# Kernel optimization log

Hardware: AMD Instinct MI355X
Metric: run time of the kernel (lower is better)

## Reference

```python
import jax, jax.numpy as jnp
import numpy as np

DIM = 256
HEADS = 8
WSZ = (2, 7, 7)
SSZ = (1, 3, 3)
EPS = 1e-5


def _rel_index(wsz):
    wt, wh, ww = wsz
    coords = np.stack(np.meshgrid(np.arange(wt), np.arange(wh), np.arange(ww), indexing='ij'))
    coords = coords.reshape(3, -1)  # (3, N)
    rel = coords[:, :, None] - coords[:, None, :]  # (3, N, N)
    rel = rel.transpose(1, 2, 0).copy()  # (N, N, 3)
    rel[:, :, 0] += wt - 1
    rel[:, :, 1] += wh - 1
    rel[:, :, 2] += ww - 1
    rel[:, :, 0] *= (2 * wh - 1) * (2 * ww - 1)
    rel[:, :, 1] *= (2 * ww - 1)
    return rel.sum(-1)  # (N, N) int


def _attn_mask_np(T, H, W, wsz, ssz):
    wt, wh, ww = wsz
    st, sh, sw = ssz
    img = np.zeros((T, H, W), np.int32)
    cnt = 0
    for t in (slice(0, -wt), slice(-wt, -st), slice(-st, None)):
        for h in (slice(0, -wh), slice(-wh, -sh), slice(-sh, None)):
            for w in (slice(0, -ww), slice(-ww, -sw), slice(-sw, None)):
                img[t, h, w] = cnt
                cnt += 1
    m = img.reshape(T // wt, wt, H // wh, wh, W // ww, ww)
    m = m.transpose(0, 2, 4, 1, 3, 5).reshape(-1, wt * wh * ww)  # (nW, N)
    diff = m[:, :, None] - m[:, None, :]
    return np.where(diff != 0, -100.0, 0.0).astype(np.float32)  # (nW, N, N)


def _ln(x, w, b):
    mu = x.mean(-1, keepdims=True)
    var = jnp.mean((x - mu) ** 2, -1, keepdims=True)
    return (x - mu) * jax.lax.rsqrt(var + EPS) * w + b


def _window_partition(x, wsz):
    B, T, H, W, C = x.shape
    wt, wh, ww = wsz
    x = x.reshape(B, T // wt, wt, H // wh, wh, W // ww, ww, C)
    x = x.transpose(0, 1, 3, 5, 2, 4, 6, 7)
    return x.reshape(-1, wt * wh * ww, C)


def _window_reverse(xw, wsz, B, T, H, W):
    wt, wh, ww = wsz
    C = xw.shape[-1]
    x = xw.reshape(B, T // wt, H // wh, W // ww, wt, wh, ww, C)
    x = x.transpose(0, 1, 4, 2, 5, 3, 6, 7)
    return x.reshape(B, T, H, W, C)


def setup_inputs() -> dict:
    key = jax.random.key(0)
    ks = jax.random.split(key, 8)
    B, T, H, W = 2, 8, 56, 56
    d = DIM
    hid = 4 * d
    rpe_rows = (2 * WSZ[0] - 1) * (2 * WSZ[1] - 1) * (2 * WSZ[2] - 1)
    s = 0.02
    return {
        'x': jax.random.normal(ks[0], (B, T, H, W, d), jnp.float32),
        'norm1_w': jnp.ones((d,), jnp.float32),
        'norm1_b': jnp.zeros((d,), jnp.float32),
        'qkv_w': jax.random.normal(ks[1], (3 * d, d), jnp.float32) * s,
        'qkv_b': jnp.zeros((3 * d,), jnp.float32),
        'proj_w': jax.random.normal(ks[2], (d, d), jnp.float32) * s,
        'proj_b': jnp.zeros((d,), jnp.float32),
        'rpe_table': jax.random.normal(ks[3], (rpe_rows, HEADS), jnp.float32) * s,
        'norm2_w': jnp.ones((d,), jnp.float32),
        'norm2_b': jnp.zeros((d,), jnp.float32),
        'fc1_w': jax.random.normal(ks[4], (hid, d), jnp.float32) * s,
        'fc1_b': jnp.zeros((hid,), jnp.float32),
        'fc2_w': jax.random.normal(ks[5], (d, hid), jnp.float32) * s,
        'fc2_b': jnp.zeros((d,), jnp.float32),
    }


def reference(x, norm1_w, norm1_b, qkv_w, qkv_b, proj_w, proj_b, rpe_table,
              norm2_w, norm2_b, fc1_w, fc1_b, fc2_w, fc2_b):
    B, T, H, W, C = x.shape
    wt, wh, ww = WSZ
    N = wt * wh * ww
    hd = C // HEADS
    scale = hd ** -0.5

    shortcut = x
    h = _ln(x, norm1_w, norm1_b)
    # shifted branch: cyclic roll + mask
    h = jnp.roll(h, (-SSZ[0], -SSZ[1], -SSZ[2]), axis=(1, 2, 3))
    mask = jnp.asarray(_attn_mask_np(T, H, W, WSZ, SSZ))  # (nW, N, N)
    nW = mask.shape[0]

    xw = _window_partition(h, WSZ)  # (B*nW, N, C)
    Bw = xw.shape[0]

    qkv = xw @ qkv_w.T + qkv_b  # (Bw, N, 3C)
    qkv = qkv.reshape(Bw, N, 3, HEADS, hd).transpose(2, 0, 3, 1, 4)
    q, k, v = qkv[0], qkv[1], qkv[2]  # (Bw, H, N, hd)

    idx = _rel_index(WSZ)  # (N, N)
    bias = rpe_table[idx].transpose(2, 0, 1)  # (heads, N, N)

    attn = jnp.einsum('bhnd,bhmd->bhnm', q * scale, k) + bias[None]
    attn = attn.reshape(B, nW, HEADS, N, N) + mask[None, :, None]
    attn = jax.nn.softmax(attn, axis=-1).reshape(Bw, HEADS, N, N)

    out = jnp.einsum('bhnm,bhmd->bhnd', attn, v)
    out = out.transpose(0, 2, 1, 3).reshape(Bw, N, C)
    out = out @ proj_w.T + proj_b

    out = _window_reverse(out, WSZ, B, T, H, W)
    out = jnp.roll(out, (SSZ[0], SSZ[1], SSZ[2]), axis=(1, 2, 3))

    x = shortcut + out
    h2 = _ln(x, norm2_w, norm2_b)
    h2 = jax.nn.gelu(h2 @ fc1_w.T + fc1_b, approximate=False)
    h2 = h2 @ fc2_w.T + fc2_b
    return x + h2
```

## Files before the change

### kernel.cpp

```cpp
#include <hip/hip_runtime.h>
#include <math.h>

#define TOKENS 50176
#define NWIN   512
#define C_DIM  256

typedef __attribute__((ext_vector_type(8))) short short8;
typedef __attribute__((ext_vector_type(4))) float f32x4;

__device__ __forceinline__ unsigned short f2bf(float f) {
    unsigned int u = __builtin_bit_cast(unsigned int, f);
    u += 0x7fffu + ((u >> 16) & 1);
    return (unsigned short)(u >> 16);
}

__device__ __forceinline__ void gll16(const void* g, void* l) {
    __builtin_amdgcn_global_load_lds(
        (const __attribute__((address_space(1))) unsigned int*)g,
        (__attribute__((address_space(3))) unsigned int*)l, 16, 0, 0);
}

__device__ __forceinline__ float gelu_exact(float v) {
    float z  = v * 0.70710678118654752f;
    float az = fabsf(z);
    float t  = __builtin_amdgcn_rcpf(1.f + 0.3275911f * az);
    float p  = ((((1.061405429f * t - 1.453152027f) * t + 1.421413741f) * t
                 - 0.284496736f) * t + 0.254829592f) * t;
    float er = 1.f - p * __expf(-az * az);
    er = (z < 0.f) ? -er : er;
    return 0.5f * v * (1.f + er);
}

__device__ __forceinline__ int win_token_to_flat(int u) {
    int g = u / 98;
    int n = u - g * 98;
    int bb  = g >> 8;
    int rem = g & 255;
    int tb = rem >> 6, hb = (rem >> 3) & 7, wb = rem & 7;
    int dt = n / 49;
    int r2 = n - dt * 49;
    int dh = r2 / 7, dw = r2 - dh * 7;
    int t = tb * 2 + dt, h = hb * 7 + dh, w = wb * 7 + dw;
    int ts = (t + 1) & 7;
    int hs = h + 3; if (hs >= 56) hs -= 56;
    int wsx = w + 3; if (wsx >= 56) wsx -= 56;
    return ((bb * 8 + ts) * 56 + hs) * 56 + wsx;
}

__global__ __launch_bounds__(256) void cvt_all_kernel(
        const float* __restrict__ s0, const float* __restrict__ s1,
        const float* __restrict__ s2, const float* __restrict__ s3,
        unsigned short* __restrict__ d0, unsigned short* __restrict__ d1,
        unsigned short* __restrict__ d2, unsigned short* __restrict__ d3) {
    int i = blockIdx.x * 256 + threadIdx.x;
    if (i < 196608)      d0[i] = f2bf(s0[i]);
    else if (i < 262144) d1[i - 196608] = f2bf(s1[i - 196608]);
    else if (i < 524288) d2[i - 262144] = f2bf(s2[i - 262144]);
    else                 d3[i - 524288] = f2bf(s3[i - 524288]);
}

__global__ __launch_bounds__(256) void bm_kernel(
        const float* __restrict__ rpe, float* __restrict__ bm) {
    int i = blockIdx.x * 256 + threadIdx.x;
    int c  = i % 112;
    int t1 = i / 112;
    int r  = t1 % 112;
    int t2 = t1 / 112;
    int head = t2 & 7;
    int cls  = t2 >> 3;
    float val;
    if (c >= 98) {
        val = -1e30f;
    } else if (r >= 98) {
        val = 0.f;
    } else {
        int dt = r / 49, rr = r - dt * 49, dh = rr / 7, dw = rr - dh * 7;
        int dt2 = c / 49, cc = c - dt2 * 49, dh2 = cc / 7, dw2 = cc - dh2 * 7;
        int rt  = (cls & 4) ? (dt  == 0 ? 1 : 2) : 0;
        int rh  = (cls & 2) ? (dh  <  4 ? 1 : 2) : 0;
        int rw  = (cls & 1) ? (dw  <  4 ? 1 : 2) : 0;
        int rt2 = (cls & 4) ? (dt2 == 0 ? 1 : 2) : 0;
        int rh2 = (cls & 2) ? (dh2 <  4 ? 1 : 2) : 0;
        int rw2 = (cls & 1) ? (dw2 <  4 ? 1 : 2) : 0;
        int reg1 = rt * 9 + rh * 3 + rw, reg2 = rt2 * 9 + rh2 * 3 + rw2;
        int idx = (dt - dt2 + 1) * 169 + (dh - dh2 + 6) * 13 + (dw - dw2 + 6);
        val = rpe[idx * 8 + head] + ((reg1 == reg2) ? 0.f : -100.f);
    }
    bm[i] = val;
}

template<bool GATHER>
__global__ __launch_bounds__(256) void ln_kernel(
        const float* __restrict__ x, const float* __restrict__ w,
        const float* __restrict__ b, unsigned short* __restrict__ out) {
    int token = blockIdx.x * 4 + (threadIdx.x >> 6);
    int lane  = threadIdx.x & 63;
    size_t so = GATHER ? (size_t)win_token_to_flat(token) * C_DIM
                       : (size_t)token * C_DIM;
    const float* src = x + so;
    float v[4];
    float sum = 0.f;
#pragma unroll
    for (int j = 0; j < 4; ++j) { v[j] = src[lane + 64 * j]; sum += v[j]; }
#pragma unroll
    for (int o = 32; o > 0; o >>= 1) sum += __shfl_xor(sum, o, 64);
    float mu = sum * (1.f / 256.f);
    float var = 0.f;
#pragma unroll
    for (int j = 0; j < 4; ++j) { float d = v[j] - mu; var += d * d; }
#pragma unroll
    for (int o = 32; o > 0; o >>= 1) var += __shfl_xor(var, o, 64);
    float rstd = rsqrtf(var * (1.f / 256.f) + 1e-5f);
    unsigned short* dst = out + (size_t)token * C_DIM;
#pragma unroll
    for (int j = 0; j < 4; ++j) {
        int c = lane + 64 * j;
        dst[c] = f2bf((v[j] - mu) * rstd * w[c] + b[c]);
    }
}

template<int EPI>
__global__ __launch_bounds__(256) void mfma_gemm(
        const unsigned short* __restrict__ A, const unsigned short* __restrict__ B,
        const float* __restrict__ bias, const float* __restrict__ res,
        void* __restrict__ Cout, int M, int N, int K) {
    __shared__ __attribute__((aligned(16))) unsigned short smem[4][128 * 32];
#define ASMB(b) (smem[(b)])
#define BSMB(b) (smem[2 + (b)])
    int tid = threadIdx.x;
    int wave = tid >> 6, lane = tid & 63;

    int nwg = gridDim.x * gridDim.y;
    int bid = blockIdx.y * gridDim.x + blockIdx.x;
    int swz = (bid & 7) * (nwg >> 3) + (bid >> 3);
    int bx = swz % gridDim.x, by = swz / gridDim.x;

    int row0 = by * 128, col0 = bx * 128;
    int wr = (wave >> 1) * 64;
    int wc = (wave & 1) * 64;

    f32x4 acc[4][4] = {};

    int sr = tid >> 2;
    int sk = (tid & 3) * 8;
    const unsigned short* Ag0 = A + (size_t)(row0 + sr) * K + sk;
    const unsigned short* Ag1 = A + (size_t)(row0 + 64 + sr) * K + sk;
    const unsigned short* Bg0 = B + (size_t)(col0 + sr) * K + sk;
    const unsigned short* Bg1 = B + (size_t)(col0 + 64 + sr) * K + sk;
    int loff = tid * 8;

    int fm = lane & 15, fq = lane >> 4;
    int fks = fq * 8;

    gll16(Ag0, &ASMB(0)[loff]);
    gll16(Ag1, &ASMB(0)[loff + 2048]);
    gll16(Bg0, &BSMB(0)[loff]);
    gll16(Bg1, &BSMB(0)[loff + 2048]);

    int nk = K >> 5;
    for (int s = 0; s < nk; ++s) {
        int cur = s & 1;
        __syncthreads();
        if (s + 1 < nk) {
            int k0 = (s + 1) << 5;
            gll16(Ag0 + k0, &ASMB(cur ^ 1)[loff]);
            gll16(Ag1 + k0, &ASMB(cur ^ 1)[loff + 2048]);
            gll16(Bg0 + k0, &BSMB(cur ^ 1)[loff]);
            gll16(Bg1 + k0, &BSMB(cur ^ 1)[loff + 2048]);
        }
        short8 af[4], bfr[4];
#pragma unroll
        for (int t4 = 0; t4 < 4; ++t4) {
            af[t4]  = *(const short8*)&ASMB(cur)[(wr + t4 * 16 + fm) * 32 + fks];
            bfr[t4] = *(const short8*)&BSMB(cur)[(wc + t4 * 16 + fm) * 32 + fks];
        }
#pragma unroll
        for (int i = 0; i < 4; ++i)
#pragma unroll
            for (int j = 0; j < 4; ++j)
                acc[i][j] = __builtin_amdgcn_mfma_f32_16x16x32_bf16(
                    af[i], bfr[j], acc[i][j], 0, 0, 0);
    }

    int ccol0 = col0 + wc + fm;
    float bj[4];
#pragma unroll
    for (int j = 0; j < 4; ++j) bj[j] = bias[ccol0 + j * 16];

    __syncthreads();

    if (EPI == 0 || EPI == 2) {
        unsigned short* Ls = &smem[0][0];
        float mul = (EPI == 0 && col0 < 256) ? 0.17677669529663687f : 1.f;
#pragma unroll
        for (int i = 0; i < 4; ++i)
#pragma unroll
            for (int v = 0; v < 4; ++v) {
                int lr = wr + i * 16 + fq * 4 + v;
#pragma unroll
                for (int j = 0; j < 4; ++j) {
                    float val = acc[i][j][v] + bj[j];
                    val = (EPI == 2) ? gelu_exact(val) : val * mul;
                    Ls[lr * 128 + wc + j * 16 + fm] = f2bf(val);
                }
            }
        __syncthreads();
        unsigned short* C = (unsigned short*)Cout;
#pragma unroll
        for (int p = 0; p < 8; ++p) {
            int lin = p * 2048 + tid * 8;
            int lr = lin >> 7, lc = lin & 127;
            *(short8*)(C + (size_t)(row0 + lr) * N + col0 + lc) =
                *(const short8*)&Ls[lin];
        }
    } else {
        float* fs = (float*)&smem[0][0];
        float* C = (float*)Cout;
#pragma unroll
        for (int h = 0; h < 2; ++h) {
            if (h) __syncthreads();
            if (wr == h * 64) {
#pragma unroll
                for (int i = 0; i < 4; ++i)
#pragma unroll
                    for (int v = 0; v < 4; ++v) {
                        int lr = i * 16 + fq * 4 + v;
#pragma unroll
                        for (int j = 0; j < 4; ++j)
                            fs[lr * 128 + wc + j * 16 + fm] = acc[i][j][v] + bj[j];
                    }
            }
            __syncthreads();
            int tr = tid >> 2, tcb = (tid & 3) * 32;
            int grow = row0 + h * 64 + tr;
            size_t gbase = (EPI == 1)
                ? (size_t)win_token_to_flat(grow) * C_DIM + col0 + tcb
                : (size_t)grow * N + col0 + tcb;
            const float* rs = res + gbase;
            float* Cp = C + gbase;
            const float* ls = &fs[tr * 128 + tcb];
#pragma unroll
            for (int q = 0; q < 8; ++q) {
                f32x4 r = *(const f32x4*)(rs + q * 4);
                f32x4 a = *(const f32x4*)(ls + q * 4);
                r.x += a.x; r.y += a.y; r.z += a.z; r.w += a.w;
                *(f32x4*)(Cp + q * 4) = r;
            }
        }
    }
#undef ASMB
#undef BSMB
}

__global__ __launch_bounds__(256) void attn_mfma_kernel(
        const unsigned short* __restrict__ qkv, const float* __restrict__ bm,
        unsigned short* __restrict__ out) {
    __shared__ __attribute__((aligned(16))) unsigned short Vt[32][136];
    __shared__ __attribute__((aligned(16))) unsigned short Pw[4][16][136];
    int blk = blockIdx.x;
    int g = blk >> 3, head = blk & 7;
    int tid = threadIdx.x, wave = tid >> 6, lane = tid & 63;

    for (int i = tid; i < 32 * 30; i += 256) {
        int d = i / 30, c = 98 + (i - d * 30);
        Vt[d][c] = 0;
    }
    const unsigned short* vbase = qkv + (size_t)g * 98 * 768 + 512 + head * 32;
    for (int i = tid; i < 98 * 16; i += 256) {
        int n = i >> 4, dp = i & 15;
        unsigned int val = *(const unsigned int*)(vbase + (size_t)n * 768 + dp * 2);
        Vt[dp * 2][n]     = (unsigned short)val;
        Vt[dp * 2 + 1][n] = (unsigned short)(val >> 16);
    }
    {
        int m = lane >> 2, c = 112 + (lane & 3) * 4;
        *(unsigned long long*)&Pw[wave][m][c] = 0ULL;
    }
    __syncthreads();

    const unsigned short* qbase = qkv + (size_t)g * 98 * 768 + head * 32;
    const unsigned short* kbase = qbase + 256;
    int rem = g & 255;
    int cls = (((rem >> 6) == 3) << 2) | (((((rem >> 3) & 7)) == 7) << 1) | ((rem & 7) == 7);
    const float* bmh = bm + (size_t)(cls * 8 + head) * 112 * 112;

    int fm = lane & 15, fq = lane >> 4;
    int fk = fq * 8;
    unsigned short* obase = out + (size_t)g * 98 * 256 + head * 32;

    for (int s = wave; s < 7; s += 4) {
        int m0 = s * 16;
        int arow = m0 + fm; if (arow > 97) arow = 97;
        short8 af = *(const short8*)(qbase + (size_t)arow * 768 + fk);
        f32x4 S[7];
        f32x4 z = {0.f, 0.f, 0.f, 0.f};
#pragma unroll
        for (int j = 0; j < 7; ++j) {
            int krow = j * 16 + fm; if (krow > 97) krow = 97;
            short8 kf = *(const short8*)(kbase + (size_t)krow * 768 + fk);
            S[j] = __builtin_amdgcn_mfma_f32_16x16x32_bf16(af, kf, z, 0, 0, 0);
        }
        const float* bmrow = bmh + (m0 + fq * 4) * 112 + fm;
#pragma unroll
        for (int j = 0; j < 7; ++j)
#pragma unroll
            for (int v = 0; v < 4; ++v)
                S[j][v] += bmrow[v * 112 + j * 16];
        float inv[4];
#pragma unroll
        for (int v = 0; v < 4; ++v) {
            float m_ = S[0][v];
#pragma unroll
            for (int j = 1; j < 7; ++j) m_ = fmaxf(m_, S[j][v]);
#pragma unroll
            for (int o = 1; o < 16; o <<= 1) m_ = fmaxf(m_, __shfl_xor(m_, o, 64));
            float t = 0.f;
#pragma unroll
            for (int j = 0; j < 7; ++j) { S[j][v] = __expf(S[j][v] - m_); t += S[j][v]; }
#pragma unroll
            for (int o = 1; o < 16; o <<= 1) t += __shfl_xor(t, o, 64);
            inv[v] = 1.f / t;
        }
#pragma unroll
        for (int j = 0; j < 7; ++j)
#pragma unroll
            for (int v = 0; v < 4; ++v)
                Pw[wave][fq * 4 + v][j * 16 + fm] = f2bf(S[j][v]);
        f32x4 O0 = {0.f, 0.f, 0.f, 0.f}, O1 = {0.f, 0.f, 0.f, 0.f};
#pragma unroll
        for (int ks = 0; ks < 4; ++ks) {
            short8 pf = *(const short8*)&Pw[wave][fm][ks * 32 + fk];
            short8 v0 = *(const short8*)&Vt[fm][ks * 32 + fk];
            short8 v1 = *(const short8*)&Vt[16 + fm][ks * 32 + fk];
            O0 = __builtin_amdgcn_mfma_f32_16x16x32_bf16(pf, v0, O0, 0, 0, 0);
            O1 = __builtin_amdgcn_mfma_f32_16x16x32_bf16(pf, v1, O1, 0, 0, 0);
        }
#pragma unroll
        for (int v = 0; v < 4; ++v) {
            int row = m0 + fq * 4 + v;
            if (row < 98) {
                obase[(size_t)row * 256 + fm]      = f2bf(O0[v] * inv[v]);
                obase[(size_t)row * 256 + 16 + fm] = f2bf(O1[v] * inv[v]);
            }
        }
    }
}

extern "C" void kernel_launch(void* const* d_in, const int* in_sizes, int n_in,
                              void* d_out, int out_size, void* d_ws, size_t ws_size,
                              hipStream_t stream) {
    const float* x     = (const float*)d_in[0];
    const float* n1w   = (const float*)d_in[1];
    const float* n1b   = (const float*)d_in[2];
    const float* qkvw  = (const float*)d_in[3];
    const float* qkvb  = (const float*)d_in[4];
    const float* projw = (const float*)d_in[5];
    const float* projb = (const float*)d_in[6];
    const float* rpe   = (const float*)d_in[7];
    const float* n2w   = (const float*)d_in[8];
    const float* n2b   = (const float*)d_in[9];
    const float* fc1w  = (const float*)d_in[10];
    const float* fc1b  = (const float*)d_in[11];
    const float* fc2w  = (const float*)d_in[12];
    const float* fc2b  = (const float*)d_in[13];
    float* out = (float*)d_out;

    unsigned short* wqkv  = (unsigned short*)d_ws;
    unsigned short* wproj = wqkv + 768 * 256;
    unsigned short* wfc1  = wproj + 256 * 256;
    unsigned short* wfc2  = wfc1 + 1024 * 256;
    float* bm = (float*)(wfc2 + 256 * 1024);
    unsigned short* actA  = (unsigned short*)(bm + 8 * 8 * 112 * 112);
    unsigned short* attnO = actA + (size_t)TOKENS * 256;
    unsigned short* qkv_bf = attnO + (size_t)TOKENS * 256;
    unsigned short* fc1o = qkv_bf;

    bm_kernel<<<8 * 8 * 112 * 112 / 256, 256, 0, stream>>>(rpe, bm);
    cvt_all_kernel<<<786432 / 256, 256, 0, stream>>>(
        qkvw, projw, fc1w, fc2w, wqkv, wproj, wfc1, wfc2);

    ln_kernel<true><<<TOKENS / 4, 256, 0, stream>>>(x, n1w, n1b, actA);
    mfma_gemm<0><<<dim3(768 / 128, TOKENS / 128), 256, 0, stream>>>(
        actA, wqkv, qkvb, nullptr, qkv_bf, TOKENS, 768, 256);
    attn_mfma_kernel<<<NWIN * 8, 256, 0, stream>>>(qkv_bf, bm, attnO);
    mfma_gemm<1><<<dim3(256 / 128, TOKENS / 128), 256, 0, stream>>>(
        attnO, wproj, projb, x, out, TOKENS, 256, 256);
    ln_kernel<false><<<TOKENS / 4, 256, 0, stream>>>(out, n2w, n2b, actA);
    mfma_gemm<2><<<dim3(1024 / 128, TOKENS / 128), 256, 0, stream>>>(
        actA, wfc1, fc1b, nullptr, fc1o, TOKENS, 1024, 256);
    mfma_gemm<3><<<dim3(256 / 128, TOKENS / 128), 256, 0, stream>>>(
        fc1o, wfc2, fc2b, out, out, TOKENS, 256, 1024);
}
```

Measured before the change: 382.5 us.

## Fuse fc1, GELU and fc2 into one MLP kernel keeping hidden activations in LDS

Replaces the two separate GEMM launches for fc1 (with GELU) and fc2 (with residual) with a single kernel. Each 64-row block computes the 1024-wide hidden layer in chunks of 128 and stores GELU results as bf16 in LDS. It then accumulates the fc2 product in registers and adds bias and residual at the end. This removes the write and re-read of the large bf16 hidden tensor through global memory. In exchange it uses 64-row tiles with a large accumulator set, more LDS, fewer waves per block and less weight reuse per tile. The generic GEMM epilogue is simplified to drop the now-unused EPI 2/3 paths.

```diff
diff --git a/kernel.cpp b/kernel.cpp
--- a/kernel.cpp
+++ b/kernel.cpp
@@ -189,20 +189,17 @@
 
     __syncthreads();
 
-    if (EPI == 0 || EPI == 2) {
+    if (EPI == 0) {
         unsigned short* Ls = &smem[0][0];
-        float mul = (EPI == 0 && col0 < 256) ? 0.17677669529663687f : 1.f;
+        float mul = (col0 < 256) ? 0.17677669529663687f : 1.f;
 #pragma unroll
         for (int i = 0; i < 4; ++i)
 #pragma unroll
             for (int v = 0; v < 4; ++v) {
                 int lr = wr + i * 16 + fq * 4 + v;
 #pragma unroll
-                for (int j = 0; j < 4; ++j) {
-                    float val = acc[i][j][v] + bj[j];
-                    val = (EPI == 2) ? gelu_exact(val) : val * mul;
-                    Ls[lr * 128 + wc + j * 16 + fm] = f2bf(val);
-                }
+                for (int j = 0; j < 4; ++j)
+                    Ls[lr * 128 + wc + j * 16 + fm] = f2bf((acc[i][j][v] + bj[j]) * mul);
             }
         __syncthreads();
         unsigned short* C = (unsigned short*)Cout;
@@ -233,9 +230,7 @@
             __syncthreads();
             int tr = tid >> 2, tcb = (tid & 3) * 32;
             int grow = row0 + h * 64 + tr;
-            size_t gbase = (EPI == 1)
-                ? (size_t)win_token_to_flat(grow) * C_DIM + col0 + tcb
-                : (size_t)grow * N + col0 + tcb;
+            size_t gbase = (size_t)win_token_to_flat(grow) * C_DIM + col0 + tcb;
             const float* rs = res + gbase;
             float* Cp = C + gbase;
             const float* ls = &fs[tr * 128 + tcb];
@@ -250,6 +245,148 @@
     }
 #undef ASMB
 #undef BSMB
+}
+
+__global__ __launch_bounds__(256, 2) void mlp_kernel(
+        const unsigned short* __restrict__ A,
+        const unsigned short* __restrict__ W1,
+        const float* __restrict__ b1,
+        const unsigned short* __restrict__ W2,
+        const float* __restrict__ b2,
+        float* __restrict__ out) {
+    __shared__ __attribute__((aligned(16))) unsigned short L[36864];
+    int tid = threadIdx.x;
+    int wave = tid >> 6, lane = tid & 63;
+    int fm = lane & 15, fq = lane >> 4;
+
+    int nwg = gridDim.x;
+    int bid = blockIdx.x;
+    int swz = (bid & 7) * (nwg >> 3) + (bid >> 3);
+    int r0 = swz * 64;
+
+    int wr  = (wave >> 1) * 32;
+    int wch = wave & 1;
+
+    int srow = tid >> 2, sk = (tid & 3) * 8;
+    const unsigned short* Ag  = A  + (size_t)(r0 + srow) * 256 + sk;
+    const unsigned short* W2s = W2 + (size_t)srow * 1024 + sk;
+
+    f32x4 acc2[2][8] = {};
+
+    for (int nc = 0; nc < 8; ++nc) {
+        const unsigned short* Bg = W1 + (size_t)(nc * 128 + srow) * 256 + sk;
+        float bj1[4];
+#pragma unroll
+        for (int j = 0; j < 4; ++j) bj1[j] = b1[nc * 128 + wch * 64 + j * 16 + fm];
+
+        gll16(Ag, &L[tid * 8]);
+        gll16(Bg, &L[4096 + tid * 8]);
+        gll16(Bg + (size_t)64 * 256, &L[4096 + 2048 + tid * 8]);
+
+        f32x4 acc1[2][4] = {};
+        for (int s = 0; s < 8; ++s) {
+            int cur = s & 1;
+            __syncthreads();
+            if (s + 1 < 8) {
+                int k0 = (s + 1) << 5;
+                gll16(Ag + k0, &L[(cur ^ 1) * 2048 + tid * 8]);
+                gll16(Bg + k0, &L[4096 + (cur ^ 1) * 4096 + tid * 8]);
+                gll16(Bg + (size_t)64 * 256 + k0,
+                      &L[4096 + (cur ^ 1) * 4096 + 2048 + tid * 8]);
+            }
+            short8 af[2], bf[4];
+#pragma unroll
+            for (int i = 0; i < 2; ++i)
+                af[i] = *(const short8*)&L[cur * 2048 + (wr + i * 16 + fm) * 32 + fq * 8];
+#pragma unroll
+            for (int j = 0; j < 4; ++j)
+                bf[j] = *(const short8*)&L[4096 + cur * 4096 +
+                                           (wch * 64 + j * 16 + fm) * 32 + fq * 8];
+#pragma unroll
+            for (int i = 0; i < 2; ++i)
+#pragma unroll
+                for (int j = 0; j < 4; ++j)
+                    acc1[i][j] = __builtin_amdgcn_mfma_f32_16x16x32_bf16(
+                        af[i], bf[j], acc1[i][j], 0, 0, 0);
+        }
+
+        {
+            int kc = nc * 128;
+#pragma unroll
+            for (int p = 0; p < 4; ++p)
+                gll16(W2s + (size_t)p * 64 * 1024 + kc,
+                      &L[20480 + p * 2048 + tid * 8]);
+        }
+#pragma unroll
+        for (int i = 0; i < 2; ++i)
+#pragma unroll
+            for (int v = 0; v < 4; ++v) {
+                int row = wr + i * 16 + fq * 4 + v;
+#pragma unroll
+                for (int j = 0; j < 4; ++j) {
+                    int col = wch * 64 + j * 16 + fm;
+                    float val = gelu_exact(acc1[i][j][v] + bj1[j]);
+                    L[12288 + (col >> 3) * 512 + row * 8 + (col & 7)] = f2bf(val);
+                }
+            }
+        __syncthreads();
+
+        for (int k2 = 0; k2 < 4; ++k2) {
+            int cb = k2 & 1;
+            if (k2) __syncthreads();
+            if (k2 + 1 < 4) {
+                int kc = nc * 128 + (k2 + 1) * 32;
+#pragma unroll
+                for (int p = 0; p < 4; ++p)
+                    gll16(W2s + (size_t)p * 64 * 1024 + kc,
+                          &L[20480 + (cb ^ 1) * 8192 + p * 2048 + tid * 8]);
+            }
+            short8 ha[2], b2f[8];
+#pragma unroll
+            for (int i = 0; i < 2; ++i)
+                ha[i] = *(const short8*)&L[12288 + (k2 * 4 + fq) * 512 +
+                                           (wr + i * 16 + fm) * 8];
+#pragma unroll
+            for (int j = 0; j < 8; ++j)
+                b2f[j] = *(const short8*)&L[20480 + cb * 8192 +
+                                            (wch * 128 + j * 16 + fm) * 32 + fq * 8];
+#pragma unroll
+            for (int i = 0; i < 2; ++i)
+#pragma unroll
+                for (int j = 0; j < 8; ++j)
+                    acc2[i][j] = __builtin_amdgcn_mfma_f32_16x16x32_bf16(
+                        ha[i], b2f[j], acc2[i][j], 0, 0, 0);
+        }
+    }
+
+    float bjo[8];
+#pragma unroll
+    for (int j = 0; j < 8; ++j) bjo[j] = b2[wch * 128 + j * 16 + fm];
+    __syncthreads();
+    float* fs = (float*)L;
+#pragma unroll
+    for (int i = 0; i < 2; ++i)
+#pragma unroll
+        for (int v = 0; v < 4; ++v) {
+            int lr = wr + i * 16 + fq * 4 + v;
+#pragma unroll
+            for (int j = 0; j < 8; ++j)
+                fs[lr * 256 + wch * 128 + j * 16 + fm] = acc2[i][j][v] + bjo[j];
+        }
+    __syncthreads();
+    {
+        int tr = tid >> 2, tcb = (tid & 3) * 64;
+        size_t gb = (size_t)(r0 + tr) * 256 + tcb;
+        const float* ls = &fs[tr * 256 + tcb];
+        float* Cp = out + gb;
+#pragma unroll
+        for (int q = 0; q < 16; ++q) {
+            f32x4 r = *(const f32x4*)(Cp + q * 4);
+            f32x4 a = *(const f32x4*)(ls + q * 4);
+            r.x += a.x; r.y += a.y; r.z += a.z; r.w += a.w;
+            *(f32x4*)(Cp + q * 4) = r;
+        }
+    }
 }
 
 __global__ __launch_bounds__(256) void attn_mfma_kernel(
@@ -373,7 +510,6 @@
     unsigned short* actA  = (unsigned short*)(bm + 8 * 8 * 112 * 112);
     unsigned short* attnO = actA + (size_t)TOKENS * 256;
     unsigned short* qkv_bf = attnO + (size_t)TOKENS * 256;
-    unsigned short* fc1o = qkv_bf;
 
     bm_kernel<<<8 * 8 * 112 * 112 / 256, 256, 0, stream>>>(rpe, bm);
     cvt_all_kernel<<<786432 / 256, 256, 0, stream>>>(
@@ -386,8 +522,6 @@
     mfma_gemm<1><<<dim3(256 / 128, TOKENS / 128), 256, 0, stream>>>(
         attnO, wproj, projb, x, out, TOKENS, 256, 256);
     ln_kernel<false><<<TOKENS / 4, 256, 0, stream>>>(out, n2w, n2b, actA);
-    mfma_gemm<2><<<dim3(1024 / 128, TOKENS / 128), 256, 0, stream>>>(
-        actA, wfc1, fc1b, nullptr, fc1o, TOKENS, 1024, 256);
-    mfma_gemm<3><<<dim3(256 / 128, TOKENS / 128), 256, 0, stream>>>(
-        fc1o, wfc2, fc2b, out, out, TOKENS, 256, 1024);
-}
+    mlp_kernel<<<TOKENS / 64, 256, 0, stream>>>(
+        actA, wfc1, fc1b, wfc2, fc2b, out);
+}
```

New measurement: 396.0 us. 1.04x slower.

## Fuse projection GEMM with residual add and LayerNorm2 in one kernel

Applied to the files above, without the earlier changes.

Replaces the projection GEMM plus separate LayerNorm kernel with a single kernel that computes full 256-column rows per 64-row tile. It adds bias and residual, writes the fp32 output, then computes row mean and variance and writes the normalized bf16 activations. This removes one kernel launch and a full fp32 re-read of the output. The cost is larger per-block tiles, more registers, smaller tiles along M, and a one-pass variance formula that is less numerically robust.

```diff
diff --git a/kernel.cpp b/kernel.cpp
--- a/kernel.cpp
+++ b/kernel.cpp
@@ -6,6 +6,7 @@
 #define C_DIM  256
 
 typedef __attribute__((ext_vector_type(8))) short short8;
+typedef __attribute__((ext_vector_type(4))) short s16x4;
 typedef __attribute__((ext_vector_type(4))) float f32x4;
 
 __device__ __forceinline__ unsigned short f2bf(float f) {
@@ -233,9 +234,7 @@
             __syncthreads();
             int tr = tid >> 2, tcb = (tid & 3) * 32;
             int grow = row0 + h * 64 + tr;
-            size_t gbase = (EPI == 1)
-                ? (size_t)win_token_to_flat(grow) * C_DIM + col0 + tcb
-                : (size_t)grow * N + col0 + tcb;
+            size_t gbase = (size_t)grow * N + col0 + tcb;
             const float* rs = res + gbase;
             float* Cp = C + gbase;
             const float* ls = &fs[tr * 128 + tcb];
@@ -250,6 +249,137 @@
     }
 #undef ASMB
 #undef BSMB
+}
+
+__global__ __launch_bounds__(256) void proj_ln_kernel(
+        const unsigned short* __restrict__ A,
+        const unsigned short* __restrict__ B,
+        const float* __restrict__ bias,
+        const float* __restrict__ res,
+        const float* __restrict__ n2w, const float* __restrict__ n2b,
+        float* __restrict__ out,
+        unsigned short* __restrict__ actA) {
+    __shared__ __attribute__((aligned(16))) unsigned short L[20480];
+    int tid = threadIdx.x;
+    int wave = tid >> 6, lane = tid & 63;
+    int fm = lane & 15, fq = lane >> 4;
+
+    int nwg = gridDim.x;
+    int bid = blockIdx.x;
+    int swz = (bid & 7) * (nwg >> 3) + (bid >> 3);
+    int r0 = swz * 64;
+
+    int wrow = (wave >> 1) * 32;
+    int wcol = (wave & 1) * 128;
+
+    f32x4 acc[2][8] = {};
+
+    int sr = tid >> 2, sk = (tid & 3) * 8;
+    const unsigned short* Ag = A + (size_t)(r0 + sr) * 256 + sk;
+    const unsigned short* Bg = B + (size_t)sr * 256 + sk;
+
+    gll16(Ag, &L[tid * 8]);
+#pragma unroll
+    for (int p = 0; p < 4; ++p)
+        gll16(Bg + (size_t)p * 16384, &L[4096 + p * 2048 + tid * 8]);
+
+    for (int s = 0; s < 8; ++s) {
+        int cur = s & 1;
+        __syncthreads();
+        if (s + 1 < 8) {
+            int k0 = (s + 1) << 5;
+            gll16(Ag + k0, &L[(cur ^ 1) * 2048 + tid * 8]);
+#pragma unroll
+            for (int p = 0; p < 4; ++p)
+                gll16(Bg + (size_t)p * 16384 + k0,
+                      &L[4096 + (cur ^ 1) * 8192 + p * 2048 + tid * 8]);
+        }
+        short8 af[2], bfr[8];
+#pragma unroll
+        for (int i = 0; i < 2; ++i)
+            af[i] = *(const short8*)&L[cur * 2048 + (wrow + i * 16 + fm) * 32 + fq * 8];
+#pragma unroll
+        for (int j = 0; j < 8; ++j)
+            bfr[j] = *(const short8*)&L[4096 + cur * 8192 +
+                                        (wcol + j * 16 + fm) * 32 + fq * 8];
+#pragma unroll
+        for (int i = 0; i < 2; ++i)
+#pragma unroll
+            for (int j = 0; j < 8; ++j)
+                acc[i][j] = __builtin_amdgcn_mfma_f32_16x16x32_bf16(
+                    af[i], bfr[j], acc[i][j], 0, 0, 0);
+    }
+
+    float bj[8];
+#pragma unroll
+    for (int j = 0; j < 8; ++j) bj[j] = bias[wcol + j * 16 + fm];
+
+    __syncthreads();
+
+    float* fs   = (float*)L;
+    float* redu = (float*)&L[16640];
+
+    int tr = tid >> 3;
+    int c0 = (tid & 7) * 4;
+
+#pragma unroll
+    for (int h = 0; h < 2; ++h) {
+        if (h) __syncthreads();
+        if (wrow == h * 32) {
+#pragma unroll
+            for (int i = 0; i < 2; ++i)
+#pragma unroll
+                for (int v = 0; v < 4; ++v) {
+                    int lr = i * 16 + fq * 4 + v;
+#pragma unroll
+                    for (int j = 0; j < 8; ++j)
+                        fs[lr * 260 + wcol + j * 16 + fm] = acc[i][j][v] + bj[j];
+                }
+        }
+        __syncthreads();
+        int flat = win_token_to_flat(r0 + h * 32 + tr);
+        size_t gb = (size_t)flat * 256;
+        float vals[32];
+        float s1 = 0.f, s2 = 0.f;
+#pragma unroll
+        for (int q = 0; q < 8; ++q) {
+            int c = c0 + q * 32;
+            f32x4 rr = *(const f32x4*)(res + gb + c);
+            f32x4 aa = *(const f32x4*)&fs[tr * 260 + c];
+            f32x4 o;
+            o.x = rr.x + aa.x; o.y = rr.y + aa.y;
+            o.z = rr.z + aa.z; o.w = rr.w + aa.w;
+            *(f32x4*)(out + gb + c) = o;
+            vals[q * 4 + 0] = o.x; vals[q * 4 + 1] = o.y;
+            vals[q * 4 + 2] = o.z; vals[q * 4 + 3] = o.w;
+            s1 += o.x + o.y + o.z + o.w;
+            s2 += o.x * o.x + o.y * o.y + o.z * o.z + o.w * o.w;
+        }
+        redu[(tr * 8 + (tid & 7)) * 2 + 0] = s1;
+        redu[(tr * 8 + (tid & 7)) * 2 + 1] = s2;
+        __syncthreads();
+        float S = 0.f, Q = 0.f;
+#pragma unroll
+        for (int g2 = 0; g2 < 8; ++g2) {
+            S += redu[(tr * 8 + g2) * 2 + 0];
+            Q += redu[(tr * 8 + g2) * 2 + 1];
+        }
+        float mu = S * (1.f / 256.f);
+        float var = Q * (1.f / 256.f) - mu * mu;
+        float rstd = rsqrtf(var + 1e-5f);
+#pragma unroll
+        for (int q = 0; q < 8; ++q) {
+            int c = c0 + q * 32;
+            f32x4 w4 = *(const f32x4*)(n2w + c);
+            f32x4 b4 = *(const f32x4*)(n2b + c);
+            s16x4 pk;
+            pk[0] = (short)f2bf((vals[q * 4 + 0] - mu) * rstd * w4.x + b4.x);
+            pk[1] = (short)f2bf((vals[q * 4 + 1] - mu) * rstd * w4.y + b4.y);
+            pk[2] = (short)f2bf((vals[q * 4 + 2] - mu) * rstd * w4.z + b4.z);
+            pk[3] = (short)f2bf((vals[q * 4 + 3] - mu) * rstd * w4.w + b4.w);
+            *(s16x4*)(actA + gb + c) = pk;
+        }
+    }
 }
 
 __global__ __launch_bounds__(256) void attn_mfma_kernel(
@@ -383,9 +513,8 @@
     mfma_gemm<0><<<dim3(768 / 128, TOKENS / 128), 256, 0, stream>>>(
         actA, wqkv, qkvb, nullptr, qkv_bf, TOKENS, 768, 256);
     attn_mfma_kernel<<<NWIN * 8, 256, 0, stream>>>(qkv_bf, bm, attnO);
-    mfma_gemm<1><<<dim3(256 / 128, TOKENS / 128), 256, 0, stream>>>(
-        attnO, wproj, projb, x, out, TOKENS, 256, 256);
-    ln_kernel<false><<<TOKENS / 4, 256, 0, stream>>>(out, n2w, n2b, actA);
+    proj_ln_kernel<<<TOKENS / 64, 256, 0, stream>>>(
+        attnO, wproj, projb, x, n2w, n2b, out, actA);
     mfma_gemm<2><<<dim3(1024 / 128, TOKENS / 128), 256, 0, stream>>>(
         actA, wfc1, fc1b, nullptr, fc1o, TOKENS, 1024, 256);
     mfma_gemm<3><<<dim3(256 / 128, TOKENS / 128), 256, 0, stream>>>(
```

Result: faster. 359.0 us (-6.1%).
